# Kernel tuning notes

Hardware: AMD Instinct MI355X
Metric: run time of the kernel (lower is better)

Reference implementation:

```python
import jax, jax.numpy as jnp
import numpy as np

ALPHA = 4.0  # spikingjelly default Sigmoid surrogate alpha
BN_EPS = 1e-5

@jax.custom_vjp
def _spike(v):
    return (v >= 0.0).astype(v.dtype)

def _spike_fwd(v):
    return _spike(v), v

def _spike_bwd(v, g):
    s = jax.nn.sigmoid(ALPHA * v)
    return (g * ALPHA * s * (1.0 - s),)

_spike.defvjp(_spike_fwd, _spike_bwd)

def lif(x, v_th):
    # Single-step LIFNode(tau=2, v_reset=0) starting from v=0:
    # v = v + (x - v)/tau = x/2 ; spike = Heaviside(v - v_th)
    return _spike(x * 0.5 - v_th)

def bn(x, p):
    # p: [4, C] = gamma, beta, running_mean, running_var (inference BN)
    g, b, m, v = p
    scale = g * jax.lax.rsqrt(v + BN_EPS)
    return x * scale[None, :, None, None] + (b - m * scale)[None, :, None, None]

def conv1x1(x, w):
    # x: [B,C,H,W], w: [O,C]
    return jnp.einsum('bchw,oc->bohw', x, w)

def dwconv3x3(x, w):
    # depthwise 3x3, w: [C,3,3]
    C = x.shape[1]
    return jax.lax.conv_general_dilated(
        x, w[:, None], (1, 1), 'SAME',
        feature_group_count=C,
        dimension_numbers=('NCHW', 'OIHW', 'NCHW'))

def branch(x, w1, dw, w2, bns):
    # RepConv: conv1x1 -> BN -> (dw3x3 -> pw1x1 -> BN), then the extra Sequential BN
    x = bn(conv1x1(x, w1), bns[0])
    x = bn(conv1x1(dwconv3x3(x, dw), w2), bns[1])
    return bn(x, bns[2])

def setup_inputs() -> dict:
    key = jax.random.key(0)
    ks = jax.random.split(key, 5)
    B, C, H, W = 16, 256, 80, 80
    x = jax.random.normal(ks[0], (B, C, H, W), jnp.float32) * 2.0  # so LIFs actually fire
    w1 = jax.random.normal(ks[1], (4, C, C), jnp.float32) * 0.06
    dw = jax.random.normal(ks[2], (4, C, 3, 3), jnp.float32) * 0.3
    w2 = jax.random.normal(ks[3], (4, C, C), jnp.float32) * 0.06
    bn_params = jax.random.uniform(ks[4], (4, 3, 4, C), jnp.float32, 0.1, 1.0)
    return {"x": x, "w1": w1, "dw": dw, "w2": w2, "bn_params": bn_params}

def reference(x, w1, dw, w2, bn_params):
    scale = 0.125
    xs = lif(x, 1.0)                                   # head_lif
    q = branch(xs, w1[0], dw[0], w2[0], bn_params[0])  # q_conv (q_lif unused in source)
    k = branch(xs, w1[1], dw[1], w2[1], bn_params[1])  # k_conv (k_lif unused in source)
    v = branch(xs, w1[2], dw[2], w2[2], bn_params[2])  # v_conv
    v = lif(v, 1.0)                                    # v_lif -> binary spikes
    # k.transpose(-2,-1) @ v : per (b,c) [W,H] @ [H,W] -> [W,W]
    kv = jnp.einsum('bchw,bchu->bcwu', k, v)
    # q @ kv : [H,W] @ [W,W] -> [H,W]
    attn = jnp.einsum('bchw,bcwu->bchu', q, kv) * scale
    s = lif(attn, 0.5)                                 # attn_lif, v_threshold=0.5
    return branch(s, w1[3], dw[3], w2[3], bn_params[3])  # proj_conv
```

## Files before the change

kernel.cpp:

```cpp
#include <hip/hip_runtime.h>
#include <hip/hip_bf16.h>
#include <cstdint>
#include <cstddef>
#include <cmath>

typedef unsigned short u16;
typedef unsigned char  u8;
typedef unsigned int   u32;
typedef __attribute__((ext_vector_type(8))) short short8;
typedef __attribute__((ext_vector_type(4))) float f32x4;
typedef __attribute__((ext_vector_type(4))) u16 u16x4;

#define CCH 256
#define HWP 6400

__device__ __forceinline__ u16 f2bf(float f) {
  u32 u = __float_as_uint(f);
  u = (u + 0x7FFFu + ((u >> 16) & 1u)) >> 16;
  return (u16)u;
}
__device__ __forceinline__ float bf2f(u16 h) { return __uint_as_float(((u32)h) << 16); }
__device__ __forceinline__ void split3(float v, u16& h, u16& m, u16& l) {
  h = f2bf(v); float r = v - bf2f(h);
  m = f2bf(r); l = f2bf(r - bf2f(m));
}
__device__ __forceinline__ void gl_lds16(const void* g, void* l) {
  __builtin_amdgcn_global_load_lds((const __attribute__((address_space(1))) unsigned int*)g,
                                   (__attribute__((address_space(3))) unsigned int*)l,
                                   16, 0, 0);
}

__global__ __launch_bounds__(256) void fold_weights(
    const float* __restrict__ w1, const float* __restrict__ w2,
    const float* __restrict__ bnp,
    u16* __restrict__ w1h, u16* __restrict__ w1m, u16* __restrict__ w1l,
    u16* __restrict__ w2h, u16* __restrict__ w2m, u16* __restrict__ w2l,
    float* __restrict__ b0f, float* __restrict__ b2f)
{
  int i = blockIdx.x >> 8, o = blockIdx.x & 255, c = threadIdx.x;
  const float* bp = bnp + i * 3072;
  double g0 = bp[0 + o],    be0 = bp[256 + o],  m0 = bp[512 + o],  v0 = bp[768 + o];
  double g1 = bp[1024 + o], be1 = bp[1280 + o], m1 = bp[1536 + o], v1 = bp[1792 + o];
  double g2 = bp[2048 + o], be2 = bp[2304 + o], m2 = bp[2560 + o], v2 = bp[2816 + o];
  double s0 = g0 / sqrt(v0 + 1e-5);
  double s1 = g1 / sqrt(v1 + 1e-5);
  double s2 = g2 / sqrt(v2 + 1e-5);
  size_t ro = (size_t)(i * 256 + o) * 256;
  float wa = (float)(s0 * (double)w1[ro + c]);
  float wb = (float)(s1 * s2 * (double)w2[ro + c]);
  u16 h, m, l;
  split3(wa, h, m, l); w1h[ro + c] = h; w1m[ro + c] = m; w1l[ro + c] = l;
  split3(wb, h, m, l); w2h[ro + c] = h; w2m[ro + c] = m; w2l[ro + c] = l;
  if (c == 0) {
    b0f[i * 256 + o] = (float)(be0 - m0 * s0);
    b2f[i * 256 + o] = (float)(s2 * (be1 - m1 * s1) + be2 - m2 * s2);
  }
}

__global__ __launch_bounds__(256) void head_spike(
    const float* __restrict__ x, u8* __restrict__ xs, int b0)
{
  __shared__ u8 tile[64][68];
  int z = blockIdx.z, c0 = blockIdx.y << 6, p0 = blockIdx.x << 6;
  int tid = threadIdx.x;
  const float* xb = x + ((size_t)(b0 + z) * CCH + c0) * HWP + p0;
#pragma unroll
  for (int j = 0; j < 16; ++j) {
    int idx = j * 256 + tid;
    int cl = idx >> 6, pl = idx & 63;
    tile[pl][cl] = (xb[(size_t)cl * HWP + pl] >= 2.0f) ? 1 : 0;
  }
  __syncthreads();
#pragma unroll
  for (int j = 0; j < 4; ++j) {
    int idx = j * 256 + tid;
    int row = idx >> 4, c4 = (idx & 15) << 2;
    *(uchar4*)(xs + ((size_t)z * HWP + p0 + row) * CCH + c0 + c4) =
        *(const uchar4*)&tile[row][c4];
  }
}

__global__ __launch_bounds__(256) void transpose_s(
    const u8* __restrict__ in, u8* __restrict__ out, int b0)
{
  __shared__ u8 tile[64][68];
  int z = blockIdx.z, c0 = blockIdx.y << 6, p0 = blockIdx.x << 6;
  int tid = threadIdx.x;
#pragma unroll
  for (int j = 0; j < 4; ++j) {
    int idx = j * 256 + tid;
    int cl = idx >> 4, p4 = (idx & 15) << 2;
    uchar4 v = *(const uchar4*)(in + ((size_t)z * CCH + c0 + cl) * HWP + p0 + p4);
    tile[p4 + 0][cl] = v.x; tile[p4 + 1][cl] = v.y;
    tile[p4 + 2][cl] = v.z; tile[p4 + 3][cl] = v.w;
  }
  __syncthreads();
#pragma unroll
  for (int j = 0; j < 4; ++j) {
    int idx = j * 256 + tid;
    int row = idx >> 4, c4 = (idx & 15) << 2;
    *(uchar4*)(out + ((size_t)(b0 + z) * HWP + p0 + row) * CCH + c0 + c4) =
        *(const uchar4*)&tile[row][c4];
  }
}

__global__ __launch_bounds__(256, 4) void gemm1(
    const u8* __restrict__ act, int b0in,
    const u16* __restrict__ WH, const u16* __restrict__ WM, const u16* __restrict__ WL,
    const float* __restrict__ bias, float* __restrict__ T1)
{
  __shared__ alignas(16) u16 As[128 * 40];
  __shared__ alignas(16) u16 LWH[4096];
  __shared__ alignas(16) u16 LWM[4096];
  __shared__ alignas(16) u16 LWL[4096];
  const int tid = threadIdx.x, wave = tid >> 6, lane = tid & 63;
  const int p0 = blockIdx.x * 128, o0 = blockIdx.y * 128, z = blockIdx.z;
  const int wm = (wave >> 1) * 64, wn = (wave & 1) * 64;
  const int lc = lane & 15, lr = lane >> 4;
  const u8* ab = act + ((size_t)(b0in + z) * HWP + p0) * CCH;
  const char* whb = (const char*)(WH + (size_t)o0 * 256);
  const char* wmb = (const char*)(WM + (size_t)o0 * 256);
  const char* wlb = (const char*)(WL + (size_t)o0 * 256);

  f32x4 acc[4][4];
#pragma unroll
  for (int i = 0; i < 4; ++i)
#pragma unroll
    for (int j = 0; j < 4; ++j) acc[i][j] = (f32x4){0.f, 0.f, 0.f, 0.f};

  const int srow = tid >> 1, shalf = tid & 1;

  for (int kc = 0; kc < 8; ++kc) {
    const int kof = kc * 64;
    __syncthreads();
#pragma unroll
    for (int t = 0; t < 2; ++t) {
      int li = t * 256 + tid;
      int row = li >> 2, ch = li & 3;
      int chp = (ch - row - (row >> 2)) & 3;
      size_t so = (size_t)row * 512 + kof + chp * 16;
      int base = (t * 256 + wave * 64) * 8;
      gl_lds16(whb + so, &LWH[base]);
      gl_lds16(wmb + so, &LWM[base]);
      gl_lds16(wlb + so, &LWL[base]);
    }
    uint4 u = *(const uint4*)(ab + (size_t)srow * CCH + kc * 32 + shalf * 16);
    u32 vv[4] = {u.x, u.y, u.z, u.w};
    u32 w[8];
#pragma unroll
    for (int q = 0; q < 4; ++q) {
      u32 v = vv[q];
      w[2 * q]     = ((v & 255u) ? 0x3F80u : 0u) | (((v >> 8) & 255u) ? 0x3F800000u : 0u);
      w[2 * q + 1] = (((v >> 16) & 255u) ? 0x3F80u : 0u) | (((v >> 24) & 255u) ? 0x3F800000u : 0u);
    }
    *(uint4*)&As[srow * 40 + shalf * 16]     = (uint4){w[0], w[1], w[2], w[3]};
    *(uint4*)&As[srow * 40 + shalf * 16 + 8] = (uint4){w[4], w[5], w[6], w[7]};
    __syncthreads();
    short8 af[4];
#pragma unroll
    for (int i = 0; i < 4; ++i)
      af[i] = *(const short8*)&As[(wm + i * 16 + lc) * 40 + lr * 8];
#pragma unroll
    for (int j = 0; j < 4; ++j) {
      int row = wn + j * 16 + lc;
      int o = row * 32 + ((lr + lc + (lc >> 2)) & 3) * 8;
      short8 bh = *(const short8*)&LWH[o];
      short8 bm = *(const short8*)&LWM[o];
      short8 bl = *(const short8*)&LWL[o];
#pragma unroll
      for (int i = 0; i < 4; ++i) {
        acc[i][j] = __builtin_amdgcn_mfma_f32_16x16x32_bf16(af[i], bl, acc[i][j], 0, 0, 0);
        acc[i][j] = __builtin_amdgcn_mfma_f32_16x16x32_bf16(af[i], bm, acc[i][j], 0, 0, 0);
        acc[i][j] = __builtin_amdgcn_mfma_f32_16x16x32_bf16(af[i], bh, acc[i][j], 0, 0, 0);
      }
    }
  }
  float* tb = T1 + ((size_t)z * HWP + p0) * CCH + o0;
#pragma unroll
  for (int j = 0; j < 4; ++j) {
    int n = wn + j * 16 + lc;
    float bn_ = bias[o0 + n];
#pragma unroll
    for (int i = 0; i < 4; ++i) {
      int m = wm + i * 16 + lr * 4;
#pragma unroll
      for (int r = 0; r < 4; ++r)
        tb[(size_t)(m + r) * CCH + n] = acc[i][j][r] + bn_;
    }
  }
}

__global__ __launch_bounds__(256) void dw3(
    const float* __restrict__ t1, const float* __restrict__ dwk,
    u16* __restrict__ oh, u16* __restrict__ om, u16* __restrict__ ol)
{
  __shared__ float lds[100 * 68];
  __shared__ float wl[576];
  const int tid = threadIdx.x;
  const int T = blockIdx.x, cg = blockIdx.y, z = blockIdx.z;
  const int ty0 = (T / 10) * 8, tx0 = (T % 10) * 8;
  const float* base = t1 + (size_t)z * HWP * CCH + cg * 64;

#pragma unroll
  for (int t = 0; t < 3; ++t) {
    int i = t * 256 + tid;
    if (i < 576) wl[i] = dwk[cg * 576 + i];
  }
#pragma unroll
  for (int t = 0; t < 7; ++t) {
    int idx = t * 256 + tid;
    if (idx < 1600) {
      int pxslot = idx >> 4;
      int c4i = (idx & 15) << 2;
      int sy = pxslot / 10, sx = pxslot - sy * 10;
      int wy = ty0 + sy - 1, wx = tx0 + sx - 1;
      float4 v = (float4){0.f, 0.f, 0.f, 0.f};
      if ((unsigned)wy < 80u && (unsigned)wx < 80u)
        v = *(const float4*)(base + (size_t)(wy * 80 + wx) * CCH + c4i);
      *(float4*)&lds[pxslot * 68 + c4i] = v;
    }
  }
  __syncthreads();

  const int cc = (tid & 15) << 2;
  const float* wc = &wl[cc * 9];
#pragma unroll
  for (int i = 0; i < 4; ++i) {
    int p_local = (tid >> 4) + i * 16;
    int ly = p_local >> 3, lx = p_local & 7;
    float a0 = 0.f, a1 = 0.f, a2 = 0.f, a3 = 0.f;
#pragma unroll
    for (int dy = -1; dy <= 1; ++dy) {
#pragma unroll
      for (int dx = -1; dx <= 1; ++dx) {
        int slot = (ly + 1 + dy) * 10 + (lx + 1 + dx);
        float4 v = *(const float4*)&lds[slot * 68 + cc];
        int t = (dy + 1) * 3 + (dx + 1);
        a0 += wc[t]      * v.x;
        a1 += wc[9 + t]  * v.y;
        a2 += wc[18 + t] * v.z;
        a3 += wc[27 + t] * v.w;
      }
    }
    u16 h0, m0, l0, h1, m1, l1, h2, m2, l2, h3, m3, l3;
    split3(a0, h0, m0, l0);
    split3(a1, h1, m1, l1);
    split3(a2, h2, m2, l2);
    split3(a3, h3, m3, l3);
    u16x4 vh, vm, vlo;
    vh.x = h0; vh.y = h1; vh.z = h2; vh.w = h3;
    vm.x = m0; vm.y = m1; vm.z = m2; vm.w = m3;
    vlo.x = l0; vlo.y = l1; vlo.z = l2; vlo.w = l3;
    int p = (ty0 + ly) * 80 + tx0 + lx;
    size_t addr = ((size_t)z * HWP + p) * CCH + cg * 64 + cc;
    *(u16x4*)(oh + addr) = vh;
    *(u16x4*)(om + addr) = vm;
    *(u16x4*)(ol + addr) = vlo;
  }
}

template <int MODE>
__global__ __launch_bounds__(256) void gemm2s(
    const u16* __restrict__ AH, const u16* __restrict__ AM, const u16* __restrict__ AL,
    const u16* __restrict__ WH, const u16* __restrict__ WM, const u16* __restrict__ WL,
    const float* __restrict__ bias, int b0,
    float* __restrict__ outF, u8* __restrict__ outB,
    u16* __restrict__ outH, u16* __restrict__ outM, u16* __restrict__ outL)
{
  __shared__ alignas(16) u16 LAH[4096];
  __shared__ alignas(16) u16 LAM[4096];
  __shared__ alignas(16) u16 LAL[4096];
  __shared__ alignas(16) u16 LWH[4096];
  __shared__ alignas(16) u16 LWM[4096];
  __shared__ alignas(16) u16 LWL[4096];
  const int tid = threadIdx.x, wave = tid >> 6, lane = tid & 63;
  const int p0 = blockIdx.x * 128, o0 = blockIdx.y * 128, z = blockIdx.z;
  const int wm = (wave >> 1) * 64, wn = (wave & 1) * 64;
  const int lc = lane & 15, lr = lane >> 4;
  const char* ahb = (const char*)(AH + ((size_t)z * HWP + p0) * 256);
  const char* amb = (const char*)(AM + ((size_t)z * HWP + p0) * 256);
  const char* alb = (const char*)(AL + ((size_t)z * HWP + p0) * 256);
  const char* whb = (const char*)(WH + (size_t)o0 * 256);
  const char* wmb = (const char*)(WM + (size_t)o0 * 256);
  const char* wlb = (const char*)(WL + (size_t)o0 * 256);

  f32x4 acc[4][4];
#pragma unroll
  for (int i = 0; i < 4; ++i)
#pragma unroll
    for (int j = 0; j < 4; ++j) acc[i][j] = (f32x4){0.f, 0.f, 0.f, 0.f};

  for (int kc = 0; kc < 8; ++kc) {
    const int kof = kc * 64;
#pragma unroll
    for (int t = 0; t < 2; ++t) {
      int li = t * 256 + tid;
      int row = li >> 2, ch = li & 3;
      int chp = (ch - row - (row >> 2)) & 3;
      size_t so = (size_t)row * 512 + kof + chp * 16;
      int base = (t * 256 + wave * 64) * 8;
      gl_lds16(ahb + so, &LAH[base]);
      gl_lds16(amb + so, &LAM[base]);
      gl_lds16(alb + so, &LAL[base]);
      gl_lds16(whb + so, &LWH[base]);
      gl_lds16(wmb + so, &LWM[base]);
      gl_lds16(wlb + so, &LWL[base]);
    }
    __syncthreads();
    short8 afH[4], afM[4], afL[4];
#pragma unroll
    for (int i = 0; i < 4; ++i) {
      int row = wm + i * 16 + lc;
      int o = row * 32 + ((lr + lc + (lc >> 2)) & 3) * 8;
      afH[i] = *(const short8*)&LAH[o];
      afM[i] = *(const short8*)&LAM[o];
      afL[i] = *(const short8*)&LAL[o];
    }
#pragma unroll
    for (int j = 0; j < 4; ++j) {
      int row = wn + j * 16 + lc;
      int o = row * 32 + ((lr + lc + (lc >> 2)) & 3) * 8;
      short8 bh = *(const short8*)&LWH[o];
      short8 bm = *(const short8*)&LWM[o];
      short8 bl = *(const short8*)&LWL[o];
#pragma unroll
      for (int i = 0; i < 4; ++i) {
        acc[i][j] = __builtin_amdgcn_mfma_f32_16x16x32_bf16(afM[i], bm, acc[i][j], 0, 0, 0);
        acc[i][j] = __builtin_amdgcn_mfma_f32_16x16x32_bf16(afL[i], bh, acc[i][j], 0, 0, 0);
        acc[i][j] = __builtin_amdgcn_mfma_f32_16x16x32_bf16(afH[i], bl, acc[i][j], 0, 0, 0);
        acc[i][j] = __builtin_amdgcn_mfma_f32_16x16x32_bf16(afM[i], bh, acc[i][j], 0, 0, 0);
        acc[i][j] = __builtin_amdgcn_mfma_f32_16x16x32_bf16(afH[i], bm, acc[i][j], 0, 0, 0);
        acc[i][j] = __builtin_amdgcn_mfma_f32_16x16x32_bf16(afH[i], bh, acc[i][j], 0, 0, 0);
      }
    }
    __syncthreads();
  }
#pragma unroll
  for (int j = 0; j < 4; ++j) {
    int n = o0 + wn + j * 16 + lc;
    float bn_ = bias[n];
    size_t rowb = ((size_t)(b0 + z) * CCH + n) * HWP + p0;
#pragma unroll
    for (int i = 0; i < 4; ++i) {
      int m = wm + i * 16 + lr * 4;
      if (MODE == 0) {
        float4 o;
        o.x = acc[i][j][0] + bn_; o.y = acc[i][j][1] + bn_;
        o.z = acc[i][j][2] + bn_; o.w = acc[i][j][3] + bn_;
        *(float4*)(outF + rowb + m) = o;
      } else if (MODE == 1) {
        uchar4 o;
        o.x = (acc[i][j][0] + bn_ >= 2.0f) ? 1 : 0;
        o.y = (acc[i][j][1] + bn_ >= 2.0f) ? 1 : 0;
        o.z = (acc[i][j][2] + bn_ >= 2.0f) ? 1 : 0;
        o.w = (acc[i][j][3] + bn_ >= 2.0f) ? 1 : 0;
        *(uchar4*)(outB + rowb + m) = o;
      } else {
        u16x4 vh, vm2, vl2;
#pragma unroll
        for (int r = 0; r < 4; ++r) {
          u16 hh, mm, ll;
          split3(acc[i][j][r] + bn_, hh, mm, ll);
          vh[r] = hh; vm2[r] = mm; vl2[r] = ll;
        }
        *(u16x4*)(outH + rowb + m) = vh;
        *(u16x4*)(outM + rowb + m) = vm2;
        *(u16x4*)(outL + rowb + m) = vl2;
      }
    }
  }
}

__global__ __launch_bounds__(320) void attn_k(
    const u16* __restrict__ qh_g, const u16* __restrict__ qm_g, const u16* __restrict__ ql_g,
    const u16* __restrict__ kh_g, const u16* __restrict__ km_g, const u16* __restrict__ kl_g,
    const u8* __restrict__ vv, u8* __restrict__ s)
{
  __shared__ alignas(16) u16 L[24960];
  __shared__ alignas(16) u8  VT[8320];
  const int tid = threadIdx.x, wave = tid >> 6, lane = tid & 63;
  const int lc = lane & 15, lr = lane >> 4;
  const size_t off = (size_t)blockIdx.x * HWP;
  u16* KH = L; u16* KM = L + 8320; u16* KL = L + 16640;

  short8 qfr[3][3];
  const int hrow = wave * 16 + lc;
#pragma unroll
  for (int kc = 0; kc < 3; ++kc) {
    int w0 = kc * 32 + lr * 8;
    if (w0 < 80) {
      size_t qo = off + (size_t)hrow * 80 + w0;
      qfr[kc][0] = *(const short8*)(qh_g + qo);
      qfr[kc][1] = *(const short8*)(qm_g + qo);
      qfr[kc][2] = *(const short8*)(ql_g + qo);
    } else {
      qfr[kc][0] = (short8){0, 0, 0, 0, 0, 0, 0, 0};
      qfr[kc][1] = qfr[kc][0];
      qfr[kc][2] = qfr[kc][0];
    }
  }

#pragma unroll
  for (int t = 0; t < 3; ++t) {
    int g = t * 320 + tid;
    int h = g / 12, wc = g - h * 12;
    int dst = h * 104 + wc * 8;
    if (wc < 10) {
      size_t so = off + (size_t)h * 80 + wc * 8;
      *(short8*)&KH[dst] = *(const short8*)(kh_g + so);
      *(short8*)&KM[dst] = *(const short8*)(km_g + so);
      *(short8*)&KL[dst] = *(const short8*)(kl_g + so);
    } else {
      short8 z8 = (short8){0, 0, 0, 0, 0, 0, 0, 0};
      *(short8*)&KH[dst] = z8; *(short8*)&KM[dst] = z8; *(short8*)&KL[dst] = z8;
    }
  }
  {
    int row = tid >> 2, qq = tid & 3;
    *(u32*)&VT[row * 104 + 80 + qq * 4] = 0;
  }
#pragma unroll
  for (int t = 0; t < 5; ++t) {
    int q = t * 320 + tid;
    int h = q / 20, w4 = (q - h * 20) * 4;
    uchar4 v4 = *(const uchar4*)(vv + off + (size_t)h * 80 + w4);
    VT[(w4 + 0) * 104 + h] = v4.x;
    VT[(w4 + 1) * 104 + h] = v4.y;
    VT[(w4 + 2) * 104 + h] = v4.z;
    VT[(w4 + 3) * 104 + h] = v4.w;
  }
  __syncthreads();

  f32x4 accS[5];
#pragma unroll
  for (int n = 0; n < 5; ++n) accS[n] = (f32x4){0.f, 0.f, 0.f, 0.f};
  for (int kc = 0; kc < 3; ++kc) {
#pragma unroll
    for (int n = 0; n < 5; ++n) {
      int bo = (n * 16 + lc) * 104 + kc * 32 + lr * 8;
      short8 kh_ = *(const short8*)&KH[bo];
      short8 km_ = *(const short8*)&KM[bo];
      short8 kl_ = *(const short8*)&KL[bo];
      __builtin_amdgcn_s_setprio(1);
      accS[n] = __builtin_amdgcn_mfma_f32_16x16x32_bf16(qfr[kc][0], kl_, accS[n], 0, 0, 0);
      accS[n] = __builtin_amdgcn_mfma_f32_16x16x32_bf16(qfr[kc][2], kh_, accS[n], 0, 0, 0);
      accS[n] = __builtin_amdgcn_mfma_f32_16x16x32_bf16(qfr[kc][1], km_, accS[n], 0, 0, 0);
      accS[n] = __builtin_amdgcn_mfma_f32_16x16x32_bf16(qfr[kc][1], kh_, accS[n], 0, 0, 0);
      accS[n] = __builtin_amdgcn_mfma_f32_16x16x32_bf16(qfr[kc][0], km_, accS[n], 0, 0, 0);
      accS[n] = __builtin_amdgcn_mfma_f32_16x16x32_bf16(qfr[kc][0], kh_, accS[n], 0, 0, 0);
      __builtin_amdgcn_s_setprio(0);
    }
  }
  __syncthreads();
#pragma unroll
  for (int n = 0; n < 5; ++n) {
#pragma unroll
    for (int r = 0; r < 4; ++r) {
      u16 hh, mm, ll; split3(accS[n][r], hh, mm, ll);
      int o = (wave * 16 + lr * 4 + r) * 104 + n * 16 + lc;
      KH[o] = hh; KM[o] = mm; KL[o] = ll;
    }
  }
  __syncthreads();
  f32x4 accA[5];
#pragma unroll
  for (int n = 0; n < 5; ++n) accA[n] = (f32x4){0.f, 0.f, 0.f, 0.f};
  for (int kc = 0; kc < 3; ++kc) {
    int ao = (wave * 16 + lc) * 104 + kc * 32 + lr * 8;
    short8 sh_ = *(const short8*)&KH[ao];
    short8 sm_ = *(const short8*)&KM[ao];
    short8 sl_ = *(const short8*)&KL[ao];
#pragma unroll
    for (int n = 0; n < 5; ++n) {
      const u8* vp = &VT[(n * 16 + lc) * 104 + kc * 32 + lr * 8];
      u32 b0 = *(const u32*)vp;
      u32 b1 = *(const u32*)(vp + 4);
      u32 e0 = ((b0 & 255u) ? 0x3F80u : 0u) | (((b0 >> 8) & 255u) ? 0x3F800000u : 0u);
      u32 e1 = (((b0 >> 16) & 255u) ? 0x3F80u : 0u) | (((b0 >> 24) & 255u) ? 0x3F800000u : 0u);
      u32 e2 = ((b1 & 255u) ? 0x3F80u : 0u) | (((b1 >> 8) & 255u) ? 0x3F800000u : 0u);
      u32 e3 = (((b1 >> 16) & 255u) ? 0x3F80u : 0u) | (((b1 >> 24) & 255u) ? 0x3F800000u : 0u);
      u32 vbw[4] = {e0, e1, e2, e3};
      short8 vb = *(const short8*)vbw;
      __builtin_amdgcn_s_setprio(1);
      accA[n] = __builtin_amdgcn_mfma_f32_16x16x32_bf16(sl_, vb, accA[n], 0, 0, 0);
      accA[n] = __builtin_amdgcn_mfma_f32_16x16x32_bf16(sm_, vb, accA[n], 0, 0, 0);
      accA[n] = __builtin_amdgcn_mfma_f32_16x16x32_bf16(sh_, vb, accA[n], 0, 0, 0);
      __builtin_amdgcn_s_setprio(0);
    }
  }
#pragma unroll
  for (int n = 0; n < 5; ++n)
#pragma unroll
    for (int r = 0; r < 4; ++r)
      s[off + (size_t)(wave * 16 + lr * 4 + r) * 80 + n * 16 + lc] =
          (accA[n][r] >= 8.0f) ? 1 : 0;
}

extern "C" void kernel_launch(void* const* d_in, const int* in_sizes, int n_in,
                              void* d_out, int out_size, void* d_ws, size_t ws_size,
                              hipStream_t stream)
{
  const float* x   = (const float*)d_in[0];
  const float* w1  = (const float*)d_in[1];
  const float* dwk = (const float*)d_in[2];
  const float* w2  = (const float*)d_in[3];
  const float* bnp = (const float*)d_in[4];
  float* out = (float*)d_out;
  char* ws = (char*)d_ws;

  u16* W1H = (u16*)(ws + 0);
  u16* W1M = (u16*)(ws + 524288);
  u16* W1L = (u16*)(ws + 1048576);
  u16* W2H = (u16*)(ws + 1572864);
  u16* W2M = (u16*)(ws + 2097152);
  u16* W2L = (u16*)(ws + 2621440);
  float* B0F = (float*)(ws + 3145728);
  float* B2F = (float*)(ws + 3149824);
  u8*    SPM = (u8*)(ws + 3153920);
  u8*    XS  = (u8*)(ws + 29368320);
  float* T1  = (float*)(ws + 42475520);
  u16*   KH_ = (u16*)(ws + 42475520);
  u16*   KM_ = (u16*)(ws + 68689920);
  u16*   QH_ = (u16*)(ws + 94904320);
  u16*   QM_ = (u16*)(ws + 121118720);
  u16*   QL_ = (u16*)(ws + 147333120);
  u16*   KL_ = (u16*)(ws + 173547520);
  u8*    V   = (u8*)(ws + 199761920);
  u16*   D2H = (u16*)(ws + 212869120);
  u16*   D2M = (u16*)(ws + 239083520);
  u16*   D2L = (u16*)(ws + 265297920);

  dim3 gb(256);
  fold_weights<<<dim3(1024), gb, 0, stream>>>(w1, w2, bnp,
      W1H, W1M, W1L, W2H, W2M, W2L, B0F, B2F);

  for (int c = 0; c < 2; ++c) {
    int b0 = c * 8;
    dim3 gh(100, 4, 8), gg(50, 2, 8), gd(100, 4, 8);
    head_spike<<<gh, gb, 0, stream>>>(x, XS, b0);
    gemm1<<<gg, gb, 0, stream>>>(XS, 0, W1H + 2 * 65536, W1M + 2 * 65536, W1L + 2 * 65536,
                                 B0F + 512, T1);
    dw3<<<gd, gb, 0, stream>>>(T1, dwk + 2 * 2304, D2H, D2M, D2L);
    gemm2s<1><<<gg, gb, 0, stream>>>(D2H, D2M, D2L,
                                     W2H + 2 * 65536, W2M + 2 * 65536, W2L + 2 * 65536,
                                     B2F + 512, 0, nullptr, V, nullptr, nullptr, nullptr);
    gemm1<<<gg, gb, 0, stream>>>(XS, 0, W1H + 0 * 65536, W1M + 0 * 65536, W1L + 0 * 65536,
                                 B0F + 0, T1);
    dw3<<<gd, gb, 0, stream>>>(T1, dwk + 0 * 2304, D2H, D2M, D2L);
    gemm2s<2><<<gg, gb, 0, stream>>>(D2H, D2M, D2L,
                                     W2H + 0 * 65536, W2M + 0 * 65536, W2L + 0 * 65536,
                                     B2F + 0, 0, nullptr, nullptr, QH_, QM_, QL_);
    gemm1<<<gg, gb, 0, stream>>>(XS, 0, W1H + 1 * 65536, W1M + 1 * 65536, W1L + 1 * 65536,
                                 B0F + 256, T1);
    dw3<<<gd, gb, 0, stream>>>(T1, dwk + 1 * 2304, D2H, D2M, D2L);
    gemm2s<2><<<gg, gb, 0, stream>>>(D2H, D2M, D2L,
                                     W2H + 1 * 65536, W2M + 1 * 65536, W2L + 1 * 65536,
                                     B2F + 256, 0, nullptr, nullptr, KH_, KM_, KL_);
    attn_k<<<dim3(2048), dim3(320), 0, stream>>>(QH_, QM_, QL_, KH_, KM_, KL_, V, V);
    transpose_s<<<gh, gb, 0, stream>>>(V, SPM, b0);
  }
  for (int c = 0; c < 2; ++c) {
    int b0 = c * 8;
    dim3 gg(50, 2, 8), gd(100, 4, 8);
    gemm1<<<gg, gb, 0, stream>>>(SPM, b0, W1H + 3 * 65536, W1M + 3 * 65536, W1L + 3 * 65536,
                                 B0F + 768, T1);
    dw3<<<gd, gb, 0, stream>>>(T1, dwk + 3 * 2304, D2H, D2M, D2L);
    gemm2s<0><<<gg, gb, 0, stream>>>(D2H, D2M, D2L,
                                     W2H + 3 * 65536, W2M + 3 * 65536, W2L + 3 * 65536,
                                     B2F + 768, b0, out, nullptr, nullptr, nullptr, nullptr);
  }
}
```

Before: 1.343 ms.

## Store depthwise output as fp32 and split into bf16 triples inside GEMM

The depthwise conv kernel now writes a single fp32 tensor instead of three bf16 hi/mid/lo planes. The second pointwise GEMM loads that fp32 tile into LDS with a swizzled layout and does the three-way bf16 split in registers just before the MFMAs. Store traffic from dw3 falls from 6 to 4 bytes per element, and the three separate A-plane loads become one. The cost is the split ALU work, which is repeated in each block that reads the same A tile, plus a different LDS footprint and register pressure. It also adds a launch-bounds occupancy hint and disables unrolling of the k-loop.

Result: slower. 2.720 ms (+102.6%).

```diff
diff --git a/kernel.cpp b/kernel.cpp
--- a/kernel.cpp
+++ b/kernel.cpp
@@ -192,7 +192,7 @@
 
 __global__ __launch_bounds__(256) void dw3(
     const float* __restrict__ t1, const float* __restrict__ dwk,
-    u16* __restrict__ oh, u16* __restrict__ om, u16* __restrict__ ol)
+    float* __restrict__ of)
 {
   __shared__ float lds[100 * 68];
   __shared__ float wl[576];
@@ -242,34 +242,22 @@
         a3 += wc[27 + t] * v.w;
       }
     }
-    u16 h0, m0, l0, h1, m1, l1, h2, m2, l2, h3, m3, l3;
-    split3(a0, h0, m0, l0);
-    split3(a1, h1, m1, l1);
-    split3(a2, h2, m2, l2);
-    split3(a3, h3, m3, l3);
-    u16x4 vh, vm, vlo;
-    vh.x = h0; vh.y = h1; vh.z = h2; vh.w = h3;
-    vm.x = m0; vm.y = m1; vm.z = m2; vm.w = m3;
-    vlo.x = l0; vlo.y = l1; vlo.z = l2; vlo.w = l3;
     int p = (ty0 + ly) * 80 + tx0 + lx;
     size_t addr = ((size_t)z * HWP + p) * CCH + cg * 64 + cc;
-    *(u16x4*)(oh + addr) = vh;
-    *(u16x4*)(om + addr) = vm;
-    *(u16x4*)(ol + addr) = vlo;
+    float4 o; o.x = a0; o.y = a1; o.z = a2; o.w = a3;
+    *(float4*)(of + addr) = o;
   }
 }
 
 template <int MODE>
-__global__ __launch_bounds__(256) void gemm2s(
-    const u16* __restrict__ AH, const u16* __restrict__ AM, const u16* __restrict__ AL,
+__global__ __launch_bounds__(256, 4) void gemm2s(
+    const float* __restrict__ AF,
     const u16* __restrict__ WH, const u16* __restrict__ WM, const u16* __restrict__ WL,
     const float* __restrict__ bias, int b0,
     float* __restrict__ outF, u8* __restrict__ outB,
     u16* __restrict__ outH, u16* __restrict__ outM, u16* __restrict__ outL)
 {
-  __shared__ alignas(16) u16 LAH[4096];
-  __shared__ alignas(16) u16 LAM[4096];
-  __shared__ alignas(16) u16 LAL[4096];
+  __shared__ alignas(16) float LA[4096];
   __shared__ alignas(16) u16 LWH[4096];
   __shared__ alignas(16) u16 LWM[4096];
   __shared__ alignas(16) u16 LWL[4096];
@@ -277,9 +265,7 @@
   const int p0 = blockIdx.x * 128, o0 = blockIdx.y * 128, z = blockIdx.z;
   const int wm = (wave >> 1) * 64, wn = (wave & 1) * 64;
   const int lc = lane & 15, lr = lane >> 4;
-  const char* ahb = (const char*)(AH + ((size_t)z * HWP + p0) * 256);
-  const char* amb = (const char*)(AM + ((size_t)z * HWP + p0) * 256);
-  const char* alb = (const char*)(AL + ((size_t)z * HWP + p0) * 256);
+  const char* afb = (const char*)(AF + ((size_t)z * HWP + p0) * 256);
   const char* whb = (const char*)(WH + (size_t)o0 * 256);
   const char* wmb = (const char*)(WM + (size_t)o0 * 256);
   const char* wlb = (const char*)(WL + (size_t)o0 * 256);
@@ -290,47 +276,66 @@
 #pragma unroll
     for (int j = 0; j < 4; ++j) acc[i][j] = (f32x4){0.f, 0.f, 0.f, 0.f};
 
+#pragma unroll 1
   for (int kc = 0; kc < 8; ++kc) {
-    const int kof = kc * 64;
+    const int kofa = kc * 128;
+    const int kofw = kc * 64;
+#pragma unroll
+    for (int t = 0; t < 4; ++t) {
+      int li = t * 256 + tid;
+      int row = li >> 3, g = li & 7;
+      int gp = (g - row - (row >> 2)) & 7;
+      size_t so = (size_t)row * 1024 + kofa + gp * 16;
+      gl_lds16(afb + so, &LA[(t * 256 + wave * 64) * 4]);
+    }
 #pragma unroll
     for (int t = 0; t < 2; ++t) {
       int li = t * 256 + tid;
       int row = li >> 2, ch = li & 3;
       int chp = (ch - row - (row >> 2)) & 3;
-      size_t so = (size_t)row * 512 + kof + chp * 16;
+      size_t so = (size_t)row * 512 + kofw + chp * 16;
       int base = (t * 256 + wave * 64) * 8;
-      gl_lds16(ahb + so, &LAH[base]);
-      gl_lds16(amb + so, &LAM[base]);
-      gl_lds16(alb + so, &LAL[base]);
       gl_lds16(whb + so, &LWH[base]);
       gl_lds16(wmb + so, &LWM[base]);
       gl_lds16(wlb + so, &LWL[base]);
     }
     __syncthreads();
-    short8 afH[4], afM[4], afL[4];
-#pragma unroll
-    for (int i = 0; i < 4; ++i) {
-      int row = wm + i * 16 + lc;
-      int o = row * 32 + ((lr + lc + (lc >> 2)) & 3) * 8;
-      afH[i] = *(const short8*)&LAH[o];
-      afM[i] = *(const short8*)&LAM[o];
-      afL[i] = *(const short8*)&LAL[o];
-    }
-#pragma unroll
-    for (int j = 0; j < 4; ++j) {
-      int row = wn + j * 16 + lc;
-      int o = row * 32 + ((lr + lc + (lc >> 2)) & 3) * 8;
-      short8 bh = *(const short8*)&LWH[o];
-      short8 bm = *(const short8*)&LWM[o];
-      short8 bl = *(const short8*)&LWL[o];
-#pragma unroll
-      for (int i = 0; i < 4; ++i) {
-        acc[i][j] = __builtin_amdgcn_mfma_f32_16x16x32_bf16(afM[i], bm, acc[i][j], 0, 0, 0);
-        acc[i][j] = __builtin_amdgcn_mfma_f32_16x16x32_bf16(afL[i], bh, acc[i][j], 0, 0, 0);
-        acc[i][j] = __builtin_amdgcn_mfma_f32_16x16x32_bf16(afH[i], bl, acc[i][j], 0, 0, 0);
-        acc[i][j] = __builtin_amdgcn_mfma_f32_16x16x32_bf16(afM[i], bh, acc[i][j], 0, 0, 0);
-        acc[i][j] = __builtin_amdgcn_mfma_f32_16x16x32_bf16(afH[i], bm, acc[i][j], 0, 0, 0);
-        acc[i][j] = __builtin_amdgcn_mfma_f32_16x16x32_bf16(afH[i], bh, acc[i][j], 0, 0, 0);
+#pragma unroll
+    for (int up = 0; up < 2; ++up) {
+      short8 aH[2], aM[2], aL[2];
+#pragma unroll
+      for (int u = 0; u < 2; ++u) {
+        int i = up * 2 + u;
+        int arow = wm + i * 16 + lc;
+        int f8 = (arow + (arow >> 2)) & 7;
+        int g0 = (lr * 2 + f8) & 7;
+        int g1 = (lr * 2 + 1 + f8) & 7;
+        float4 fa = *(const float4*)&LA[arow * 32 + g0 * 4];
+        float4 fb = *(const float4*)&LA[arow * 32 + g1 * 4];
+        float av[8] = {fa.x, fa.y, fa.z, fa.w, fb.x, fb.y, fb.z, fb.w};
+#pragma unroll
+        for (int e = 0; e < 8; ++e) {
+          u16 hh, mm, ll; split3(av[e], hh, mm, ll);
+          aH[u][e] = (short)hh; aM[u][e] = (short)mm; aL[u][e] = (short)ll;
+        }
+      }
+#pragma unroll
+      for (int j = 0; j < 4; ++j) {
+        int row = wn + j * 16 + lc;
+        int o = row * 32 + ((lr + lc + (lc >> 2)) & 3) * 8;
+        short8 bh = *(const short8*)&LWH[o];
+        short8 bm = *(const short8*)&LWM[o];
+        short8 bl = *(const short8*)&LWL[o];
+#pragma unroll
+        for (int u = 0; u < 2; ++u) {
+          int i = up * 2 + u;
+          acc[i][j] = __builtin_amdgcn_mfma_f32_16x16x32_bf16(aM[u], bm, acc[i][j], 0, 0, 0);
+          acc[i][j] = __builtin_amdgcn_mfma_f32_16x16x32_bf16(aL[u], bh, acc[i][j], 0, 0, 0);
+          acc[i][j] = __builtin_amdgcn_mfma_f32_16x16x32_bf16(aH[u], bl, acc[i][j], 0, 0, 0);
+          acc[i][j] = __builtin_amdgcn_mfma_f32_16x16x32_bf16(aM[u], bh, acc[i][j], 0, 0, 0);
+          acc[i][j] = __builtin_amdgcn_mfma_f32_16x16x32_bf16(aH[u], bm, acc[i][j], 0, 0, 0);
+          acc[i][j] = __builtin_amdgcn_mfma_f32_16x16x32_bf16(aH[u], bh, acc[i][j], 0, 0, 0);
+        }
       }
     }
     __syncthreads();
@@ -526,9 +531,7 @@
   u16*   QL_ = (u16*)(ws + 147333120);
   u16*   KL_ = (u16*)(ws + 173547520);
   u8*    V   = (u8*)(ws + 199761920);
-  u16*   D2H = (u16*)(ws + 212869120);
-  u16*   D2M = (u16*)(ws + 239083520);
-  u16*   D2L = (u16*)(ws + 265297920);
+  float* D2F = (float*)(ws + 212869120);
 
   dim3 gb(256);
   fold_weights<<<dim3(1024), gb, 0, stream>>>(w1, w2, bnp,
@@ -540,20 +543,20 @@
     head_spike<<<gh, gb, 0, stream>>>(x, XS, b0);
     gemm1<<<gg, gb, 0, stream>>>(XS, 0, W1H + 2 * 65536, W1M + 2 * 65536, W1L + 2 * 65536,
                                  B0F + 512, T1);
-    dw3<<<gd, gb, 0, stream>>>(T1, dwk + 2 * 2304, D2H, D2M, D2L);
-    gemm2s<1><<<gg, gb, 0, stream>>>(D2H, D2M, D2L,
+    dw3<<<gd, gb, 0, stream>>>(T1, dwk + 2 * 2304, D2F);
+    gemm2s<1><<<gg, gb, 0, stream>>>(D2F,
                                      W2H + 2 * 65536, W2M + 2 * 65536, W2L + 2 * 65536,
                                      B2F + 512, 0, nullptr, V, nullptr, nullptr, nullptr);
     gemm1<<<gg, gb, 0, stream>>>(XS, 0, W1H + 0 * 65536, W1M + 0 * 65536, W1L + 0 * 65536,
                                  B0F + 0, T1);
-    dw3<<<gd, gb, 0, stream>>>(T1, dwk + 0 * 2304, D2H, D2M, D2L);
-    gemm2s<2><<<gg, gb, 0, stream>>>(D2H, D2M, D2L,
+    dw3<<<gd, gb, 0, stream>>>(T1, dwk + 0 * 2304, D2F);
+    gemm2s<2><<<gg, gb, 0, stream>>>(D2F,
                                      W2H + 0 * 65536, W2M + 0 * 65536, W2L + 0 * 65536,
                                      B2F + 0, 0, nullptr, nullptr, QH_, QM_, QL_);
     gemm1<<<gg, gb, 0, stream>>>(XS, 0, W1H + 1 * 65536, W1M + 1 * 65536, W1L + 1 * 65536,
                                  B0F + 256, T1);
-    dw3<<<gd, gb, 0, stream>>>(T1, dwk + 1 * 2304, D2H, D2M, D2L);
-    gemm2s<2><<<gg, gb, 0, stream>>>(D2H, D2M, D2L,
+    dw3<<<gd, gb, 0, stream>>>(T1, dwk + 1 * 2304, D2F);
+    gemm2s<2><<<gg, gb, 0, stream>>>(D2F,
                                      W2H + 1 * 65536, W2M + 1 * 65536, W2L + 1 * 65536,
                                      B2F + 256, 0, nullptr, nullptr, KH_, KM_, KL_);
     attn_k<<<dim3(2048), dim3(320), 0, stream>>>(QH_, QM_, QL_, KH_, KM_, KL_, V, V);
@@ -564,8 +567,8 @@
     dim3 gg(50, 2, 8), gd(100, 4, 8);
     gemm1<<<gg, gb, 0, stream>>>(SPM, b0, W1H + 3 * 65536, W1M + 3 * 65536, W1L + 3 * 65536,
                                  B0F + 768, T1);
-    dw3<<<gd, gb, 0, stream>>>(T1, dwk + 3 * 2304, D2H, D2M, D2L);
-    gemm2s<0><<<gg, gb, 0, stream>>>(D2H, D2M, D2L,
+    dw3<<<gd, gb, 0, stream>>>(T1, dwk + 3 * 2304, D2F);
+    gemm2s<0><<<gg, gb, 0, stream>>>(D2F,
                                      W2H + 3 * 65536, W2M + 3 * 65536, W2L + 3 * 65536,
                                      B2F + 768, b0, out, nullptr, nullptr, nullptr, nullptr);
   }
```
